# Optimization experiments

Hardware: AMD Instinct MI355X
Metric: run time of the kernel (lower is better)

## Reference

```python
import jax, jax.numpy as jnp
import numpy as np

N = 2_000_000
VOXEL_SIZE = (0.1, 0.1, 0.1)
PC_RANGE = (-50.0, -50.0, -5.0, 50.0, 50.0, 3.0)
NUM_BATCHES = 4


def setup_inputs() -> dict:
    key = jax.random.key(0)
    k1, k2 = jax.random.split(key)
    pmin = jnp.array(PC_RANGE[:3], dtype=jnp.float32)
    pmax = jnp.array(PC_RANGE[3:], dtype=jnp.float32)
    # points uniformly distributed over the configured point-cloud range
    points = jax.random.uniform(k1, (N, 3), dtype=jnp.float32, minval=pmin, maxval=pmax)
    batch_indices = jnp.sort(jax.random.randint(k2, (N,), 0, NUM_BATCHES, dtype=jnp.int32))
    return {"points": points, "batch_indices": batch_indices}


def reference(points, batch_indices):
    """Vectorized equivalent of PointVoxelizer.forward.

    Returns fixed-shape (jit-friendly) analogues of the torch outputs:
      voxel_coords   [N, 4] int32  [batch, z, y, x], padded rows = -1
      voxel_features [N, 3] float32 voxel centers, padded rows = 0
      point_to_voxel_map [N] int32, -1 for invalid points
      n_voxels       scalar int32, number of real (non-padding) voxels
    The per-batch torch.unique + offset concatenation is reproduced exactly by
    a single sorted unique over the combined hash batch*GRID + cell_hash,
    since unique sorts and the hash is lexicographic in (batch, x, y, z).
    """
    dtype = points.dtype
    vsize = jnp.array(VOXEL_SIZE, dtype=dtype)
    pmin = jnp.array(PC_RANGE[:3], dtype=dtype)
    pmax = jnp.array(PC_RANGE[3:], dtype=dtype)

    vc = jnp.floor((points - pmin) / vsize).astype(jnp.int32)  # [N,3] (x,y,z)
    grid = jnp.ceil((pmax - pmin) / vsize).astype(jnp.int32)   # [3] = (1000,1000,80)
    valid = jnp.all(vc >= 0, axis=1) & jnp.all(vc < grid, axis=1)  # [N]

    YZ = grid[1] * grid[2]
    GXYZ = grid[0] * YZ  # cells per batch element (8e7 < 2^31/NUM_BATCHES)
    cell_hash = vc[:, 0] * YZ + vc[:, 1] * grid[2] + vc[:, 2]
    SENTINEL = jnp.iinfo(jnp.int32).max
    combined = jnp.where(valid, batch_indices.astype(jnp.int32) * GXYZ + cell_hash, SENTINEL)

    uniq, inv = jnp.unique(combined, return_inverse=True, size=N, fill_value=SENTINEL)
    is_real = uniq != SENTINEL  # padding (and any invalid-point bucket) masked out

    point_to_voxel_map = jnp.where(valid, inv.reshape(-1).astype(jnp.int32), -1)

    b = uniq // GXYZ
    rem = uniq % GXYZ
    x = rem // YZ
    y = (rem % YZ) // grid[2]
    z = rem % grid[2]

    coords_bzyx = jnp.stack([b, z, y, x], axis=1).astype(jnp.int32)  # [N,4]
    voxel_coords = jnp.where(is_real[:, None], coords_bzyx, -1)

    xyz = jnp.stack([x, y, z], axis=1).astype(dtype)
    centers = pmin + (xyz + 0.5) * vsize
    voxel_features = jnp.where(is_real[:, None], centers, jnp.zeros((), dtype))

    n_voxels = is_real.sum().astype(jnp.int32)
    return voxel_coords, voxel_features, point_to_voxel_map, n_voxels
```

## Files before the change

kernel.cpp:

```cpp
#include <hip/hip_runtime.h>


namespace {

constexpr int GX = 1000, GY = 1000, GZ = 80;
constexpr int YZ = GY * GZ;
constexpr int GXYZ = GX * YZ;
constexpr int TOTAL_CELLS = GXYZ * 4;
constexpr int BBITS = 18;
constexpr int BCELLS = 1 << BBITS;
constexpr int NB = (TOTAL_CELLS + BCELLS - 1) >> BBITS;
constexpr int BWORDS = BCELLS / 32;
constexpr int NCHUNK = 1024;
static_assert(NCHUNK % 64 == 0, "k2a wave scan");

constexpr size_t OFF_PK   = 8000000;
constexpr size_t OFF_HIST = 24000000;
constexpr size_t OFF_TOT  = 30000000;
constexpr size_t OFF_BOFF = 30100000;
constexpr size_t OFF_DCNT = 30200000;

__global__ void k1_keys_hist(const float* __restrict__ pts, const int* __restrict__ bi,
                             unsigned* __restrict__ upt, unsigned* __restrict__ hist,
                             float* __restrict__ out_map, int n, int cpb) {
  __shared__ unsigned h[NB];
  const int c = blockIdx.x;
  for (int b = threadIdx.x; b < NB; b += blockDim.x) h[b] = 0;
  __syncthreads();
  const int lo = c * cpb, hi = min(n, lo + cpb);
  for (int i = lo + threadIdx.x; i < hi; i += blockDim.x) {
    float px = pts[3 * i + 0], py = pts[3 * i + 1], pz = pts[3 * i + 2];
    int vx = (int)floorf((px + 50.0f) / 0.1f);
    int vy = (int)floorf((py + 50.0f) / 0.1f);
    int vz = (int)floorf((pz + 5.0f) / 0.1f);
    bool valid = (vx >= 0) & (vy >= 0) & (vz >= 0) & (vx < GX) & (vy < GY) & (vz < GZ);
    unsigned u = 0xFFFFFFFFu;
    if (valid) {
      u = (unsigned)(bi[i] * GXYZ + vx * YZ + vy * GZ + vz);
      atomicAdd(&h[u >> BBITS], 1u);
    } else {
      out_map[i] = -1.0f;
    }
    upt[i] = u;
  }
  __syncthreads();
  for (int b = threadIdx.x; b < NB; b += blockDim.x)
    hist[(size_t)c * NB + b] = h[b];
}

__global__ void k2a_chunk_pre(unsigned* __restrict__ hist, unsigned* __restrict__ tot) {
  const int wid = (blockIdx.x * blockDim.x + threadIdx.x) >> 6;
  const int lane = threadIdx.x & 63;
  if (wid >= NB) return;
  unsigned run = 0;
  for (int c0 = 0; c0 < NCHUNK; c0 += 64) {
    const size_t idx = (size_t)(c0 + lane) * NB + wid;
    unsigned v = hist[idx];
    unsigned inc = v;
    for (int o = 1; o < 64; o <<= 1) {
      unsigned t = __shfl_up(inc, o);
      if (lane >= o) inc += t;
    }
    hist[idx] = run + inc - v;
    run += __shfl(inc, 63);
  }
  if (lane == 63) tot[wid] = run;
}

__global__ void k2b_scan_tot(const unsigned* __restrict__ tot, unsigned* __restrict__ boff) {
  __shared__ unsigned s[1024];
  const int tid = threadIdx.x;
  unsigned v0 = (2 * tid     < NB) ? tot[2 * tid]     : 0u;
  unsigned v1 = (2 * tid + 1 < NB) ? tot[2 * tid + 1] : 0u;
  unsigned t = v0 + v1;
  s[tid] = t;
  __syncthreads();
  for (int o = 1; o < 1024; o <<= 1) {
    unsigned add = (tid >= o) ? s[tid - o] : 0u;
    __syncthreads();
    s[tid] += add;
    __syncthreads();
  }
  unsigned excl = s[tid] - t;
  if (2 * tid     < NB) boff[2 * tid]     = excl;
  if (2 * tid + 1 < NB) boff[2 * tid + 1] = excl + v0;
  if (tid == 1023) boff[NB] = s[1023];
}

__global__ void k3_scatter(const unsigned* __restrict__ upt, const unsigned* __restrict__ hist,
                           const unsigned* __restrict__ boff, unsigned long long* __restrict__ pk,
                           int n, int cpb) {
  __shared__ unsigned cur[NB];
  const int c = blockIdx.x;
  for (int b = threadIdx.x; b < NB; b += blockDim.x)
    cur[b] = boff[b] + hist[(size_t)c * NB + b];
  __syncthreads();
  const int lo = c * cpb, hi = min(n, lo + cpb);
  for (int i = lo + threadIdx.x; i < hi; i += blockDim.x) {
    unsigned u = upt[i];
    if (u == 0xFFFFFFFFu) continue;
    unsigned p = atomicAdd(&cur[u >> BBITS], 1u);
    pk[p] = ((unsigned long long)u << 32) | (unsigned)i;
  }
}

__global__ void __launch_bounds__(1024) k4_count(const unsigned long long* __restrict__ pk,
                                                 const unsigned* __restrict__ boff,
                                                 unsigned* __restrict__ dcnt) {
  __shared__ unsigned bits[BWORDS];
  __shared__ unsigned red[1024];
  const int b = blockIdx.x, tid = threadIdx.x;
  for (int w = tid; w < BWORDS; w += 1024) bits[w] = 0;
  __syncthreads();
  const unsigned lo = boff[b], hi = boff[b + 1];
  const unsigned base = (unsigned)b << BBITS;
  for (unsigned p = lo + tid; p < hi; p += 1024) {
    unsigned local = (unsigned)(pk[p] >> 32) - base;
    atomicOr(&bits[local >> 5], 1u << (local & 31));
  }
  __syncthreads();
  unsigned cnt = 0;
  for (int w = tid; w < BWORDS; w += 1024) cnt += __popc(bits[w]);
  red[tid] = cnt;
  __syncthreads();
  for (int o = 512; o > 0; o >>= 1) {
    if (tid < o) red[tid] += red[tid + o];
    __syncthreads();
  }
  if (tid == 0) dcnt[b] = red[0];
}

__global__ void __launch_bounds__(1024) k6_emit(
    const unsigned long long* __restrict__ pk, const unsigned* __restrict__ boff,
    const unsigned* __restrict__ dcnt, float* __restrict__ out_coords,
    float* __restrict__ out_feats, float* __restrict__ out_map,
    float* __restrict__ out_nvox, int n) {
  __shared__ unsigned bits[BWORDS];
  __shared__ unsigned wpre[BWORDS];
  __shared__ unsigned s[1024];
  const int tid = threadIdx.x;
  const int bid = blockIdx.x;

  if (bid >= NB) {
    unsigned part = 0;
    for (int k = tid; k < NB; k += 1024) part += dcnt[k];
    s[tid] = part;
    __syncthreads();
    for (int o = 512; o > 0; o >>= 1) {
      if (tid < o) s[tid] += s[tid + o];
      __syncthreads();
    }
    const unsigned nv = s[0];
    if (bid == NB && tid == 0) *out_nvox = (float)nv;
    const int row = (bid - NB) * 1024 + tid;
    if (row < n && (unsigned)row >= nv) {
      float* c = out_coords + (size_t)row * 4;
      c[0] = -1.0f; c[1] = -1.0f; c[2] = -1.0f; c[3] = -1.0f;
      float* f = out_feats + (size_t)row * 3;
      f[0] = 0.0f; f[1] = 0.0f; f[2] = 0.0f;
    }
    return;
  }

  unsigned part = 0;
  for (int k = tid; k < bid; k += 1024) part += dcnt[k];
  s[tid] = part;
  __syncthreads();
  for (int o = 512; o > 0; o >>= 1) {
    if (tid < o) s[tid] += s[tid + o];
    __syncthreads();
  }
  const unsigned drank = s[0];
  __syncthreads();

  for (int w = tid; w < BWORDS; w += 1024) bits[w] = 0;
  __syncthreads();
  const unsigned lo = boff[bid], hi = boff[bid + 1];
  const unsigned base = (unsigned)bid << BBITS;
  for (unsigned p = lo + tid; p < hi; p += 1024) {
    unsigned local = (unsigned)(pk[p] >> 32) - base;
    atomicOr(&bits[local >> 5], 1u << (local & 31));
  }
  __syncthreads();

  const int wb = tid * 8;
  unsigned c8[8];
  unsigned t = 0;
  #pragma unroll
  for (int j = 0; j < 8; j++) {
    unsigned p = __popc(bits[wb + j]);
    c8[j] = t;
    t += p;
  }
  s[tid] = t;
  __syncthreads();
  for (int o = 1; o < 1024; o <<= 1) {
    unsigned add = (tid >= o) ? s[tid - o] : 0u;
    __syncthreads();
    s[tid] += add;
    __syncthreads();
  }
  const unsigned excl = s[tid] - t;
  #pragma unroll
  for (int j = 0; j < 8; j++) wpre[wb + j] = excl + c8[j];
  __syncthreads();

  #pragma unroll
  for (int j = 0; j < 8; j++) {
    const int w = wb + j;
    unsigned m = bits[w];
    unsigned r = drank + wpre[w];
    const unsigned lbase = (unsigned)w << 5;
    while (m) {
      int bit = __ffs(m) - 1;
      m &= m - 1;
      unsigned u = base + lbase + (unsigned)bit;
      int bat = (int)(u / (unsigned)GXYZ);
      int rem = (int)(u % (unsigned)GXYZ);
      int x = rem / YZ, ry = rem % YZ;
      int y = ry / GZ, z = ry % GZ;
      float* cc = out_coords + (size_t)r * 4;
      cc[0] = (float)bat; cc[1] = (float)z; cc[2] = (float)y; cc[3] = (float)x;
      float* ff = out_feats + (size_t)r * 3;
      ff[0] = -50.0f + ((float)x + 0.5f) * 0.1f;
      ff[1] = -50.0f + ((float)y + 0.5f) * 0.1f;
      ff[2] = -5.0f + ((float)z + 0.5f) * 0.1f;
      r++;
    }
  }

  for (unsigned p = lo + tid; p < hi; p += 1024) {
    unsigned long long e = pk[p];
    unsigned local = (unsigned)(e >> 32) - base;
    unsigned w = local >> 5;
    unsigned r = drank + wpre[w] + (unsigned)__popc(bits[w] & ((1u << (local & 31)) - 1u));
    out_map[(unsigned)e] = (float)r;
  }
}

}

extern "C" void kernel_launch(void* const* d_in, const int* in_sizes, int n_in,
                              void* d_out, int out_size, void* d_ws, size_t ws_size,
                              hipStream_t stream) {
  const int N = in_sizes[0] / 3;
  const float* pts = (const float*)d_in[0];
  const int* bi = (const int*)d_in[1];
  float* out = (float*)d_out;

  unsigned* upt = (unsigned*)d_ws;
  unsigned long long* pk = (unsigned long long*)((char*)d_ws + OFF_PK);
  unsigned* hist = (unsigned*)((char*)d_ws + OFF_HIST);
  unsigned* tot  = (unsigned*)((char*)d_ws + OFF_TOT);
  unsigned* boff = (unsigned*)((char*)d_ws + OFF_BOFF);
  unsigned* dcnt = (unsigned*)((char*)d_ws + OFF_DCNT);

  float* out_coords = out;
  float* out_feats  = out + 4LL * N;
  float* out_map    = out + 7LL * N;
  float* out_nvox   = out + 8LL * N;

  const int cpb = (N + NCHUNK - 1) / NCHUNK;
  const int pad_blocks = (N + 1023) / 1024;

  k1_keys_hist<<<NCHUNK, 256, 0, stream>>>(pts, bi, upt, hist, out_map, N, cpb);
  k2a_chunk_pre<<<(NB * 64 + 255) / 256, 256, 0, stream>>>(hist, tot);
  k2b_scan_tot<<<1, 1024, 0, stream>>>(tot, boff);
  k3_scatter<<<NCHUNK, 256, 0, stream>>>(upt, hist, boff, pk, N, cpb);
  k4_count<<<NB, 1024, 0, stream>>>(pk, boff, dcnt);
  k6_emit<<<NB + pad_blocks, 1024, 0, stream>>>(pk, boff, dcnt, out_coords,
                                                out_feats, out_map, out_nvox, N);
}
```

Before: 194.5 us.

## Split packed key/index into 32-bit arrays and gather point map via separate kernel

The 64-bit key|index scatter buffer is replaced by a 32-bit key array plus a per-point position array. k6 now writes ranks contiguously in sorted order, and a new k7 kernel gathers them back per point. This turns k6's random scattered map writes into coalesced writes and halves key traffic in k4/k6, at the cost of an extra kernel launch and a random-read gather. The shared-memory bitmap is also swizzled so the per-thread popcount scan reads bank-conflict-free.

After: 197.9 us. No clear change (+1.7%).

```diff
diff --git a/kernel.cpp b/kernel.cpp
--- a/kernel.cpp
+++ b/kernel.cpp
@@ -15,14 +15,20 @@
 static_assert(NCHUNK % 64 == 0, "k2a wave scan");
 
 constexpr size_t OFF_PK   = 8000000;
-constexpr size_t OFF_HIST = 24000000;
-constexpr size_t OFF_TOT  = 30000000;
-constexpr size_t OFF_BOFF = 30100000;
-constexpr size_t OFF_DCNT = 30200000;
+constexpr size_t OFF_POS  = 16000000;
+constexpr size_t OFF_MVAL = 24000000;
+constexpr size_t OFF_HIST = 32000000;
+constexpr size_t OFF_TOT  = 38000000;
+constexpr size_t OFF_BOFF = 38100000;
+constexpr size_t OFF_DCNT = 38200000;
+
+__device__ __forceinline__ int sw(int w) {
+  return ((w & 7) << 10) | (w >> 3);
+}
 
 __global__ void k1_keys_hist(const float* __restrict__ pts, const int* __restrict__ bi,
                              unsigned* __restrict__ upt, unsigned* __restrict__ hist,
-                             float* __restrict__ out_map, int n, int cpb) {
+                             int n, int cpb) {
   __shared__ unsigned h[NB];
   const int c = blockIdx.x;
   for (int b = threadIdx.x; b < NB; b += blockDim.x) h[b] = 0;
@@ -38,8 +44,6 @@
     if (valid) {
       u = (unsigned)(bi[i] * GXYZ + vx * YZ + vy * GZ + vz);
       atomicAdd(&h[u >> BBITS], 1u);
-    } else {
-      out_map[i] = -1.0f;
     }
     upt[i] = u;
   }
@@ -88,8 +92,8 @@
 }
 
 __global__ void k3_scatter(const unsigned* __restrict__ upt, const unsigned* __restrict__ hist,
-                           const unsigned* __restrict__ boff, unsigned long long* __restrict__ pk,
-                           int n, int cpb) {
+                           const unsigned* __restrict__ boff, unsigned* __restrict__ pk,
+                           unsigned* __restrict__ pos, int n, int cpb) {
   __shared__ unsigned cur[NB];
   const int c = blockIdx.x;
   for (int b = threadIdx.x; b < NB; b += blockDim.x)
@@ -100,11 +104,12 @@
     unsigned u = upt[i];
     if (u == 0xFFFFFFFFu) continue;
     unsigned p = atomicAdd(&cur[u >> BBITS], 1u);
-    pk[p] = ((unsigned long long)u << 32) | (unsigned)i;
-  }
-}
-
-__global__ void __launch_bounds__(1024) k4_count(const unsigned long long* __restrict__ pk,
+    pk[p] = u;
+    pos[i] = p;
+  }
+}
+
+__global__ void __launch_bounds__(1024) k4_count(const unsigned* __restrict__ pk,
                                                  const unsigned* __restrict__ boff,
                                                  unsigned* __restrict__ dcnt) {
   __shared__ unsigned bits[BWORDS];
@@ -115,7 +120,7 @@
   const unsigned lo = boff[b], hi = boff[b + 1];
   const unsigned base = (unsigned)b << BBITS;
   for (unsigned p = lo + tid; p < hi; p += 1024) {
-    unsigned local = (unsigned)(pk[p] >> 32) - base;
+    unsigned local = pk[p] - base;
     atomicOr(&bits[local >> 5], 1u << (local & 31));
   }
   __syncthreads();
@@ -131,9 +136,9 @@
 }
 
 __global__ void __launch_bounds__(1024) k6_emit(
-    const unsigned long long* __restrict__ pk, const unsigned* __restrict__ boff,
+    const unsigned* __restrict__ pk, const unsigned* __restrict__ boff,
     const unsigned* __restrict__ dcnt, float* __restrict__ out_coords,
-    float* __restrict__ out_feats, float* __restrict__ out_map,
+    float* __restrict__ out_feats, float* __restrict__ mapval,
     float* __restrict__ out_nvox, int n) {
   __shared__ unsigned bits[BWORDS];
   __shared__ unsigned wpre[BWORDS];
@@ -178,17 +183,16 @@
   const unsigned lo = boff[bid], hi = boff[bid + 1];
   const unsigned base = (unsigned)bid << BBITS;
   for (unsigned p = lo + tid; p < hi; p += 1024) {
-    unsigned local = (unsigned)(pk[p] >> 32) - base;
-    atomicOr(&bits[local >> 5], 1u << (local & 31));
-  }
-  __syncthreads();
-
-  const int wb = tid * 8;
+    unsigned local = pk[p] - base;
+    atomicOr(&bits[sw(local >> 5)], 1u << (local & 31));
+  }
+  __syncthreads();
+
   unsigned c8[8];
   unsigned t = 0;
   #pragma unroll
   for (int j = 0; j < 8; j++) {
-    unsigned p = __popc(bits[wb + j]);
+    unsigned p = __popc(bits[j * 1024 + tid]);
     c8[j] = t;
     t += p;
   }
@@ -202,15 +206,15 @@
   }
   const unsigned excl = s[tid] - t;
   #pragma unroll
-  for (int j = 0; j < 8; j++) wpre[wb + j] = excl + c8[j];
+  for (int j = 0; j < 8; j++) wpre[j * 1024 + tid] = excl + c8[j];
   __syncthreads();
 
   #pragma unroll
   for (int j = 0; j < 8; j++) {
-    const int w = wb + j;
-    unsigned m = bits[w];
-    unsigned r = drank + wpre[w];
-    const unsigned lbase = (unsigned)w << 5;
+    const int slot = j * 1024 + tid;
+    unsigned m = bits[slot];
+    unsigned r = drank + wpre[slot];
+    const unsigned lbase = (unsigned)(tid * 8 + j) << 5;
     while (m) {
       int bit = __ffs(m) - 1;
       m &= m - 1;
@@ -230,12 +234,23 @@
   }
 
   for (unsigned p = lo + tid; p < hi; p += 1024) {
-    unsigned long long e = pk[p];
-    unsigned local = (unsigned)(e >> 32) - base;
-    unsigned w = local >> 5;
-    unsigned r = drank + wpre[w] + (unsigned)__popc(bits[w] & ((1u << (local & 31)) - 1u));
-    out_map[(unsigned)e] = (float)r;
-  }
+    unsigned local = pk[p] - base;
+    int slot = sw((int)(local >> 5));
+    unsigned r = drank + wpre[slot] + (unsigned)__popc(bits[slot] & ((1u << (local & 31)) - 1u));
+    mapval[p] = (float)r;
+  }
+}
+
+__global__ void k7_map(const unsigned* __restrict__ upt, const unsigned* __restrict__ pos,
+                       const float* __restrict__ mapval, float* __restrict__ out_map, int n) {
+  int i = blockIdx.x * blockDim.x + threadIdx.x;
+  if (i >= n) return;
+  unsigned u = upt[i];
+  if (u == 0xFFFFFFFFu) {
+    out_map[i] = -1.0f;
+    return;
+  }
+  out_map[i] = mapval[pos[i]];
 }
 
 }
@@ -249,7 +264,9 @@
   float* out = (float*)d_out;
 
   unsigned* upt = (unsigned*)d_ws;
-  unsigned long long* pk = (unsigned long long*)((char*)d_ws + OFF_PK);
+  unsigned* pk   = (unsigned*)((char*)d_ws + OFF_PK);
+  unsigned* pos  = (unsigned*)((char*)d_ws + OFF_POS);
+  float*    mval = (float*)((char*)d_ws + OFF_MVAL);
   unsigned* hist = (unsigned*)((char*)d_ws + OFF_HIST);
   unsigned* tot  = (unsigned*)((char*)d_ws + OFF_TOT);
   unsigned* boff = (unsigned*)((char*)d_ws + OFF_BOFF);
@@ -263,11 +280,12 @@
   const int cpb = (N + NCHUNK - 1) / NCHUNK;
   const int pad_blocks = (N + 1023) / 1024;
 
-  k1_keys_hist<<<NCHUNK, 256, 0, stream>>>(pts, bi, upt, hist, out_map, N, cpb);
+  k1_keys_hist<<<NCHUNK, 256, 0, stream>>>(pts, bi, upt, hist, N, cpb);
   k2a_chunk_pre<<<(NB * 64 + 255) / 256, 256, 0, stream>>>(hist, tot);
   k2b_scan_tot<<<1, 1024, 0, stream>>>(tot, boff);
-  k3_scatter<<<NCHUNK, 256, 0, stream>>>(upt, hist, boff, pk, N, cpb);
+  k3_scatter<<<NCHUNK, 256, 0, stream>>>(upt, hist, boff, pk, pos, N, cpb);
   k4_count<<<NB, 1024, 0, stream>>>(pk, boff, dcnt);
   k6_emit<<<NB + pad_blocks, 1024, 0, stream>>>(pk, boff, dcnt, out_coords,
-                                                out_feats, out_map, out_nvox, N);
-}
+                                                out_feats, mval, out_nvox, N);
+  k7_map<<<(N + 1023) / 1024, 1024, 0, stream>>>(upt, pos, mval, out_map, N);
+}
```
